# Kernel optimization log

Hardware: AMD Instinct MI355X
Metric: run time of the kernel (lower is better)

## Reference

```python
import math
import jax, jax.numpy as jnp
import numpy as np

N_TYPES = 4
TYPE_DIMS = [64, 128, 96, 32]   # in_features per type (matches init type_dims)
OUT_DIM = 256
N_VERTS = 500_000
MAX_FEAT = max(TYPE_DIMS)       # 128, padded feature width


def setup_inputs() -> dict:
    key = jax.random.key(0)
    ks = jax.random.split(key, 2 + 2 * N_TYPES)
    inp = {
        "features": jax.random.normal(ks[0], (N_VERTS, MAX_FEAT), dtype=jnp.float32),
        "type_ids": jax.random.randint(ks[1], (N_VERTS,), 0, N_TYPES, dtype=jnp.int64),
    }
    # Per-type Linear params, PyTorch-style init: U(-1/sqrt(in), 1/sqrt(in)).
    for t, d in enumerate(TYPE_DIMS):
        bound = 1.0 / math.sqrt(d)
        inp[f"W{t}"] = jax.random.uniform(ks[2 + 2 * t], (d, OUT_DIM), dtype=jnp.float32,
                                          minval=-bound, maxval=bound)
        inp[f"b{t}"] = jax.random.uniform(ks[3 + 2 * t], (OUT_DIM,), dtype=jnp.float32,
                                          minval=-bound, maxval=bound)
    return inp


def reference(features, type_ids, W0, b0, W1, b1, W2, b2, W3, b3):
    # features: (N, MAX_FEAT), type_ids: (N,) -> out: (N, OUT_DIM)
    Ws = [W0, W1, W2, W3]
    bs = [b0, b1, b2, b3]
    out = jnp.zeros((features.shape[0], OUT_DIM), dtype=features.dtype)
    for t in range(N_TYPES):
        d = Ws[t].shape[0]
        # Linear on the first in_dim columns (rest is padding), as in the torch module.
        y = features[:, :d] @ Ws[t] + bs[t]            # (N, OUT_DIM)
        out = jnp.where((type_ids == t)[:, None], y, out)
    return out
```

## Files before the change

kernel.cpp:

```cpp
#include <hip/hip_runtime.h>


typedef __attribute__((ext_vector_type(8))) __bf16 bf16x8;
typedef __attribute__((ext_vector_type(4))) __bf16 bf16x4;
typedef __attribute__((ext_vector_type(4))) float f32x4;

#define WS_WBUF_BYTES 2000128

__global__ void count_kernel(const int* __restrict__ types, int n,
                             int* __restrict__ counts) {
    __shared__ int h[4];
    if (threadIdx.x < 4) h[threadIdx.x] = 0;
    __syncthreads();
    for (int i = blockIdx.x * blockDim.x + threadIdx.x; i < n;
         i += gridDim.x * blockDim.x)
        atomicAdd(&h[types[i]], 1);
    __syncthreads();
    if (threadIdx.x < 4) atomicAdd(&counts[threadIdx.x], h[threadIdx.x]);
}

__global__ void bases_kernel(const int* __restrict__ counts,
                             int* __restrict__ bases, int* __restrict__ cursors) {
    if (threadIdx.x == 0) {
        int s = 0;
        for (int t = 0; t < 4; ++t) { bases[t] = s; cursors[t] = s; s += counts[t]; }
    }
}

__global__ void scatter_kernel(const int* __restrict__ types, int n,
                               int* __restrict__ cursors, int* __restrict__ idx) {
    __shared__ int h[4], hb[4], cur[4];
    const int tid = threadIdx.x;
    if (tid < 4) h[tid] = 0;
    __syncthreads();
    const int i0 = blockIdx.x * 1024;
    int myt[4];
    #pragma unroll
    for (int k = 0; k < 4; ++k) {
        int i = i0 + k * 256 + tid;
        myt[k] = (i < n) ? types[i] : -1;
        if (myt[k] >= 0) atomicAdd(&h[myt[k]], 1);
    }
    __syncthreads();
    if (tid < 4) { hb[tid] = atomicAdd(&cursors[tid], h[tid]); cur[tid] = 0; }
    __syncthreads();
    #pragma unroll
    for (int k = 0; k < 4; ++k) {
        if (myt[k] >= 0) {
            int p = atomicAdd(&cur[myt[k]], 1);
            idx[hb[myt[k]] + p] = i0 + k * 256 + tid;
        }
    }
}

__global__ void wswz_kernel(const float* __restrict__ W0, const float* __restrict__ W1,
                            const float* __restrict__ W2, const float* __restrict__ W3,
                            __bf16* __restrict__ wbuf) {
    int o = blockIdx.x * 256 + threadIdx.x;
    if (o >= 81920) return;
    const int woff[5] = {0, 16384, 49152, 73728, 81920};
    int t = 0;
    while (o >= woff[t + 1]) ++t;
    int rel = o - woff[t];
    int j    = rel & 7;
    int lane = (rel >> 3) & 63;
    int cb   = rel >> 9;
    int c    = cb >> 4;
    int nt   = cb & 15;
    int k = c * 32 + (lane >> 4) * 8 + j;
    int n = nt * 16 + (lane & 15);
    const float* W = (t == 0) ? W0 : (t == 1) ? W1 : (t == 2) ? W2 : W3;
    wbuf[o] = (__bf16)W[k * 256 + n];
}

template <int TT, int K, int WOFF>
__launch_bounds__(256, 3)
__global__ void gemm_kernel(const float* __restrict__ feat,
                            const int* __restrict__ ws_i,
                            const __bf16* __restrict__ wbuf,
                            const float* __restrict__ bias,
                            float* __restrict__ out) {
    const int cnt = ws_i[TT];
    const int m0  = (int)blockIdx.x * 64;
    if (m0 >= cnt) return;
    const int base = ws_i[8 + TT];
    const int* __restrict__ idxbuf = ws_i + 16;
    const int mcount = min(64, cnt - m0);

    constexpr int LDA = K + 8;
    __shared__ __bf16 ldsA[64 * LDA];
    __shared__ float  ldsOut[16 * 260];
    __shared__ int    lidx[64];

    const int tid = threadIdx.x;
    if (tid < 64) lidx[tid] = (tid < mcount) ? idxbuf[base + m0 + tid] : 0;
    __syncthreads();

    constexpr int K4 = K / 4;
    for (int f = tid; f < 64 * K4; f += 256) {
        int row = f / K4;
        int c4  = f - row * K4;
        if (row < mcount) {
            int g = lidx[row];
            f32x4 v = *reinterpret_cast<const f32x4*>(&feat[(size_t)g * 128 + c4 * 4]);
            bf16x4 h = {(__bf16)v.x, (__bf16)v.y, (__bf16)v.z, (__bf16)v.w};
            *reinterpret_cast<bf16x4*>(&ldsA[row * LDA + c4 * 4]) = h;
        }
    }
    __syncthreads();

    const int lane = tid & 63;
    const int wave = tid >> 6;
    const int m = lane & 15;
    const int q = lane >> 4;

    f32x4 acc[4][4] = {};
    const __bf16* __restrict__ wb = wbuf + WOFF;

    #pragma unroll
    for (int c = 0; c < K / 32; ++c) {
        bf16x8 a[4];
        #pragma unroll
        for (int mi = 0; mi < 4; ++mi)
            a[mi] = *reinterpret_cast<const bf16x8*>(
                        &ldsA[(mi * 16 + m) * LDA + c * 32 + q * 8]);
        #pragma unroll
        for (int ni = 0; ni < 4; ++ni) {
            int nt = wave * 4 + ni;
            bf16x8 b = *reinterpret_cast<const bf16x8*>(
                           wb + ((size_t)(c * 16 + nt) * 64 + lane) * 8);
            #pragma unroll
            for (int mi = 0; mi < 4; ++mi)
                acc[mi][ni] = __builtin_amdgcn_mfma_f32_16x16x32_bf16(
                                  a[mi], b, acc[mi][ni], 0, 0, 0);
        }
    }

    const f32x4 bias4 = *reinterpret_cast<const f32x4*>(&bias[lane * 4]);

    #pragma unroll
    for (int mi = 0; mi < 4; ++mi) {
        __syncthreads();
        #pragma unroll
        for (int ni = 0; ni < 4; ++ni) {
            int col = (wave * 4 + ni) * 16 + m;
            #pragma unroll
            for (int r = 0; r < 4; ++r)
                ldsOut[(q * 4 + r) * 260 + col] = acc[mi][ni][r];
        }
        __syncthreads();
        #pragma unroll
        for (int it = 0; it < 4; ++it) {
            int r = it * 4 + wave;
            int lrow = mi * 16 + r;
            if (lrow < mcount) {
                int g = lidx[lrow];
                f32x4 v = *reinterpret_cast<const f32x4*>(&ldsOut[r * 260 + lane * 4]);
                v += bias4;
                *reinterpret_cast<f32x4*>(&out[(size_t)g * 256 + lane * 4]) = v;
            }
        }
    }
}

extern "C" void kernel_launch(void* const* d_in, const int* in_sizes, int n_in,
                              void* d_out, int out_size, void* d_ws, size_t ws_size,
                              hipStream_t stream) {
    const float* feat  = (const float*)d_in[0];
    const int*   types = (const int*)d_in[1];
    const float* W0 = (const float*)d_in[2];
    const float* b0 = (const float*)d_in[3];
    const float* W1 = (const float*)d_in[4];
    const float* b1 = (const float*)d_in[5];
    const float* W2 = (const float*)d_in[6];
    const float* b2 = (const float*)d_in[7];
    const float* W3 = (const float*)d_in[8];
    const float* b3 = (const float*)d_in[9];
    float* out = (float*)d_out;
    const int n = in_sizes[0] / 128;

    char* ws = (char*)d_ws;
    int* ws_i    = (int*)ws;
    int* counts  = ws_i;
    int* cursors = ws_i + 4;
    int* bases   = ws_i + 8;
    int* idx     = ws_i + 16;
    __bf16* wbuf = (__bf16*)(ws + WS_WBUF_BYTES);

    hipMemsetAsync(counts, 0, 48, stream);
    count_kernel<<<489, 256, 0, stream>>>(types, n, counts);
    bases_kernel<<<1, 64, 0, stream>>>(counts, bases, cursors);
    scatter_kernel<<<(n + 1023) / 1024, 256, 0, stream>>>(types, n, cursors, idx);
    wswz_kernel<<<320, 256, 0, stream>>>(W0, W1, W2, W3, wbuf);

    const int tiles = (n + 63) / 64;
    gemm_kernel<0,  64,     0><<<tiles, 256, 0, stream>>>(feat, ws_i, wbuf, b0, out);
    gemm_kernel<1, 128, 16384><<<tiles, 256, 0, stream>>>(feat, ws_i, wbuf, b1, out);
    gemm_kernel<2,  96, 49152><<<tiles, 256, 0, stream>>>(feat, ws_i, wbuf, b2, out);
    gemm_kernel<3,  32, 73728><<<tiles, 256, 0, stream>>>(feat, ws_i, wbuf, b3, out);
}
```

Measured before the change: 718.4 us.

## Fuse per-type GEMMs into one launch and write MFMA results directly

Merges the count and weight-swizzle kernels into one prep launch. The four per-type GEMM launches become a single grid, with tile-to-type offsets computed in bases_kernel, so the empty half-launches per type go away. The MFMA operands are swapped so each lane holds four consecutive output columns, and results are stored straight to global memory with bias added, dropping the LDS transpose stage and its barriers. The output stores become 16-byte chunks scattered across rows per wave instead of full contiguous rows, which may reduce write coalescing.

```diff
diff --git a/kernel.cpp b/kernel.cpp
--- a/kernel.cpp
+++ b/kernel.cpp
@@ -7,23 +7,49 @@
 
 #define WS_WBUF_BYTES 2000128
 
-__global__ void count_kernel(const int* __restrict__ types, int n,
-                             int* __restrict__ counts) {
-    __shared__ int h[4];
-    if (threadIdx.x < 4) h[threadIdx.x] = 0;
-    __syncthreads();
-    for (int i = blockIdx.x * blockDim.x + threadIdx.x; i < n;
-         i += gridDim.x * blockDim.x)
-        atomicAdd(&h[types[i]], 1);
-    __syncthreads();
-    if (threadIdx.x < 4) atomicAdd(&counts[threadIdx.x], h[threadIdx.x]);
+__global__ void prep_kernel(const int* __restrict__ types, int n,
+                            int* __restrict__ counts,
+                            const float* __restrict__ W0, const float* __restrict__ W1,
+                            const float* __restrict__ W2, const float* __restrict__ W3,
+                            __bf16* __restrict__ wbuf) {
+    if (blockIdx.x < 320) {
+        int o = blockIdx.x * 256 + threadIdx.x;
+        const int woff[5] = {0, 16384, 49152, 73728, 81920};
+        int t = 0;
+        while (o >= woff[t + 1]) ++t;
+        int rel = o - woff[t];
+        int j    = rel & 7;
+        int lane = (rel >> 3) & 63;
+        int cb   = rel >> 9;
+        int c    = cb >> 4;
+        int nt   = cb & 15;
+        int k = c * 32 + (lane >> 4) * 8 + j;
+        int nn = nt * 16 + (lane & 15);
+        const float* W = (t == 0) ? W0 : (t == 1) ? W1 : (t == 2) ? W2 : W3;
+        wbuf[o] = (__bf16)W[k * 256 + nn];
+    } else {
+        __shared__ int h[4];
+        if (threadIdx.x < 4) h[threadIdx.x] = 0;
+        __syncthreads();
+        for (int i = (int)(blockIdx.x - 320) * 256 + threadIdx.x; i < n;
+             i += 489 * 256)
+            atomicAdd(&h[types[i]], 1);
+        __syncthreads();
+        if (threadIdx.x < 4) atomicAdd(&counts[threadIdx.x], h[threadIdx.x]);
+    }
 }
 
 __global__ void bases_kernel(const int* __restrict__ counts,
-                             int* __restrict__ bases, int* __restrict__ cursors) {
+                             int* __restrict__ bases, int* __restrict__ cursors,
+                             int* __restrict__ tb) {
     if (threadIdx.x == 0) {
-        int s = 0;
-        for (int t = 0; t < 4; ++t) { bases[t] = s; cursors[t] = s; s += counts[t]; }
+        int s = 0, ts = 0;
+        for (int t = 0; t < 4; ++t) {
+            bases[t] = s; cursors[t] = s; tb[t] = ts;
+            s += counts[t];
+            ts += (counts[t] + 63) >> 6;
+        }
+        tb[4] = ts;
     }
 }
 
@@ -53,46 +79,17 @@
     }
 }
 
-__global__ void wswz_kernel(const float* __restrict__ W0, const float* __restrict__ W1,
-                            const float* __restrict__ W2, const float* __restrict__ W3,
-                            __bf16* __restrict__ wbuf) {
-    int o = blockIdx.x * 256 + threadIdx.x;
-    if (o >= 81920) return;
-    const int woff[5] = {0, 16384, 49152, 73728, 81920};
-    int t = 0;
-    while (o >= woff[t + 1]) ++t;
-    int rel = o - woff[t];
-    int j    = rel & 7;
-    int lane = (rel >> 3) & 63;
-    int cb   = rel >> 9;
-    int c    = cb >> 4;
-    int nt   = cb & 15;
-    int k = c * 32 + (lane >> 4) * 8 + j;
-    int n = nt * 16 + (lane & 15);
-    const float* W = (t == 0) ? W0 : (t == 1) ? W1 : (t == 2) ? W2 : W3;
-    wbuf[o] = (__bf16)W[k * 256 + n];
-}
-
-template <int TT, int K, int WOFF>
-__launch_bounds__(256, 3)
-__global__ void gemm_kernel(const float* __restrict__ feat,
-                            const int* __restrict__ ws_i,
-                            const __bf16* __restrict__ wbuf,
-                            const float* __restrict__ bias,
-                            float* __restrict__ out) {
-    const int cnt = ws_i[TT];
-    const int m0  = (int)blockIdx.x * 64;
-    if (m0 >= cnt) return;
-    const int base = ws_i[8 + TT];
-    const int* __restrict__ idxbuf = ws_i + 16;
-    const int mcount = min(64, cnt - m0);
-
+template <int K, int WOFF>
+__device__ __forceinline__ void gemm_body(const float* __restrict__ feat,
+                                          const int* __restrict__ idxbuf,
+                                          int base, int m0, int mcount,
+                                          const __bf16* __restrict__ wbuf,
+                                          const float* __restrict__ bias,
+                                          float* __restrict__ out,
+                                          __bf16* ldsA, int* lidx) {
     constexpr int LDA = K + 8;
-    __shared__ __bf16 ldsA[64 * LDA];
-    __shared__ float  ldsOut[16 * 260];
-    __shared__ int    lidx[64];
-
     const int tid = threadIdx.x;
+
     if (tid < 64) lidx[tid] = (tid < mcount) ? idxbuf[base + m0 + tid] : 0;
     __syncthreads();
 
@@ -132,34 +129,53 @@
             #pragma unroll
             for (int mi = 0; mi < 4; ++mi)
                 acc[mi][ni] = __builtin_amdgcn_mfma_f32_16x16x32_bf16(
-                                  a[mi], b, acc[mi][ni], 0, 0, 0);
-        }
-    }
-
-    const f32x4 bias4 = *reinterpret_cast<const f32x4*>(&bias[lane * 4]);
-
+                                  b, a[mi], acc[mi][ni], 0, 0, 0);
+        }
+    }
+
+    f32x4 biasv[4];
+    #pragma unroll
+    for (int ni = 0; ni < 4; ++ni)
+        biasv[ni] = *reinterpret_cast<const f32x4*>(&bias[wave * 64 + ni * 16 + q * 4]);
     #pragma unroll
     for (int mi = 0; mi < 4; ++mi) {
-        __syncthreads();
-        #pragma unroll
-        for (int ni = 0; ni < 4; ++ni) {
-            int col = (wave * 4 + ni) * 16 + m;
+        int v = mi * 16 + m;
+        if (v < mcount) {
+            size_t ro = (size_t)lidx[v] * 256 + wave * 64 + q * 4;
             #pragma unroll
-            for (int r = 0; r < 4; ++r)
-                ldsOut[(q * 4 + r) * 260 + col] = acc[mi][ni][r];
-        }
-        __syncthreads();
-        #pragma unroll
-        for (int it = 0; it < 4; ++it) {
-            int r = it * 4 + wave;
-            int lrow = mi * 16 + r;
-            if (lrow < mcount) {
-                int g = lidx[lrow];
-                f32x4 v = *reinterpret_cast<const f32x4*>(&ldsOut[r * 260 + lane * 4]);
-                v += bias4;
-                *reinterpret_cast<f32x4*>(&out[(size_t)g * 256 + lane * 4]) = v;
+            for (int ni = 0; ni < 4; ++ni) {
+                f32x4 r = acc[mi][ni] + biasv[ni];
+                *reinterpret_cast<f32x4*>(&out[ro + ni * 16]) = r;
             }
         }
+    }
+}
+
+__launch_bounds__(256, 3)
+__global__ void gemm_all(const float* __restrict__ feat,
+                         const int* __restrict__ ws_i,
+                         const __bf16* __restrict__ wbuf,
+                         const float* __restrict__ b0, const float* __restrict__ b1,
+                         const float* __restrict__ b2, const float* __restrict__ b3,
+                         float* __restrict__ out) {
+    __shared__ __bf16 ldsA[64 * 136];
+    __shared__ int lidx[64];
+
+    const int* tb = ws_i + 12;
+    const int blk = blockIdx.x;
+    if (blk >= tb[4]) return;
+    const int t = (blk >= tb[2]) ? ((blk >= tb[3]) ? 3 : 2)
+                                 : ((blk >= tb[1]) ? 1 : 0);
+    const int m0     = (blk - tb[t]) * 64;
+    const int mcount = min(64, ws_i[t] - m0);
+    const int base   = ws_i[8 + t];
+    const int* idxbuf = ws_i + 32;
+
+    switch (t) {
+        case 0: gemm_body< 64,     0>(feat, idxbuf, base, m0, mcount, wbuf, b0, out, ldsA, lidx); break;
+        case 1: gemm_body<128, 16384>(feat, idxbuf, base, m0, mcount, wbuf, b1, out, ldsA, lidx); break;
+        case 2: gemm_body< 96, 49152>(feat, idxbuf, base, m0, mcount, wbuf, b2, out, ldsA, lidx); break;
+        case 3: gemm_body< 32, 73728>(feat, idxbuf, base, m0, mcount, wbuf, b3, out, ldsA, lidx); break;
     }
 }
 
@@ -184,18 +200,15 @@
     int* counts  = ws_i;
     int* cursors = ws_i + 4;
     int* bases   = ws_i + 8;
-    int* idx     = ws_i + 16;
+    int* tb      = ws_i + 12;
+    int* idx     = ws_i + 32;
     __bf16* wbuf = (__bf16*)(ws + WS_WBUF_BYTES);
 
     hipMemsetAsync(counts, 0, 48, stream);
-    count_kernel<<<489, 256, 0, stream>>>(types, n, counts);
-    bases_kernel<<<1, 64, 0, stream>>>(counts, bases, cursors);
+    prep_kernel<<<809, 256, 0, stream>>>(types, n, counts, W0, W1, W2, W3, wbuf);
+    bases_kernel<<<1, 64, 0, stream>>>(counts, bases, cursors, tb);
     scatter_kernel<<<(n + 1023) / 1024, 256, 0, stream>>>(types, n, cursors, idx);
-    wswz_kernel<<<320, 256, 0, stream>>>(W0, W1, W2, W3, wbuf);
-
-    const int tiles = (n + 63) / 64;
-    gemm_kernel<0,  64,     0><<<tiles, 256, 0, stream>>>(feat, ws_i, wbuf, b0, out);
-    gemm_kernel<1, 128, 16384><<<tiles, 256, 0, stream>>>(feat, ws_i, wbuf, b1, out);
-    gemm_kernel<2,  96, 49152><<<tiles, 256, 0, stream>>>(feat, ws_i, wbuf, b2, out);
-    gemm_kernel<3,  32, 73728><<<tiles, 256, 0, stream>>>(feat, ws_i, wbuf, b3, out);
-}
+
+    const int tiles = (n + 63) / 64 + 4;
+    gemm_all<<<tiles, 256, 0, stream>>>(feat, ws_i, wbuf, b0, b1, b2, b3, out);
+}
```

After: 737.3 us. +2.6%, slower.
